# Kernel optimization log

Hardware: AMD Instinct MI355X
Metric: run time of the kernel (lower is better)

## Reference

```python
import jax, jax.numpy as jnp
import numpy as np

B, NB, NA, D, PF = 16384, 8, 16, 128, 1
IN_DIM = D + NA * D + D  # basis + flattened sf + task = 2304
QK_DIM = D * 3 * PF      # 384
V_DIM = D * PF           # 128


def rbf_similarity(x, y):
    # RBF kernel over the feature axis: exp(-0.5 * ||x - y||^2)
    return jnp.exp(-0.5 * jnp.sum((x - y) ** 2, axis=-1))


def setup_inputs() -> dict:
    key = jax.random.key(0)
    ks = jax.random.split(key, 9)
    basis = jax.random.normal(ks[0], (B, NB, D), dtype=jnp.float32)
    sf_all = jax.random.normal(ks[1], (B, NB, NA, D), dtype=jnp.float32)
    task = jax.random.normal(ks[2], (B, NB, D), dtype=jnp.float32)
    mask = (jax.random.uniform(ks[3], (B, NB, D * PF)) > 0.5).astype(jnp.float32)
    s_in = 1.0 / np.sqrt(IN_DIM)
    s_v = 1.0 / np.sqrt(D)
    Wq = jax.random.normal(ks[4], (IN_DIM, QK_DIM), dtype=jnp.float32) * s_in
    Wk = jax.random.normal(ks[5], (IN_DIM, QK_DIM), dtype=jnp.float32) * s_in
    bk = jnp.zeros((QK_DIM,), dtype=jnp.float32)
    Wv = jax.random.normal(ks[6], (D, V_DIM), dtype=jnp.float32) * s_v
    bv = jnp.zeros((V_DIM,), dtype=jnp.float32)
    return {"basis_features_all": basis, "sf_all": sf_all, "task": task, "mask": mask,
            "Wq": Wq, "Wk": Wk, "bk": bk, "Wv": Wv, "bv": bv}


def reference(basis_features_all, sf_all, task, mask, Wq, Wk, bk, Wv, bv):
    b = sf_all.shape[0]
    sf_all_r = jnp.reshape(sf_all, (b, NB, NA * D))          # (B, NB, NA*D)
    sf_first_r = sf_all_r[:, :1, :]                          # (B, 1, NA*D)
    task = jax.lax.stop_gradient(task)
    task_n = task / jnp.linalg.norm(task, ord=2, axis=-1, keepdims=True)

    # RBF similarity side-branch between consecutive beakers
    bst = jnp.concatenate([basis_features_all, sf_all_r, task_n], axis=-1)  # (B, NB, IN_DIM)
    sim = rbf_similarity(bst[:, :-1, :], bst[:, 1:, :]).mean(axis=0)        # (NB-1,)

    bf_first = basis_features_all[:, :1, :]
    bf_rest = jax.lax.stop_gradient(basis_features_all[:, 1:, :])
    bf_all = jnp.concatenate([bf_first, bf_rest], axis=1)

    q_in = jnp.concatenate([bf_first, sf_first_r, task_n[:, :1, :]], axis=-1)  # (B, 1, IN_DIM)
    query = q_in @ Wq                                                          # (B, 1, QK)
    k_in = jnp.concatenate([bf_all, sf_all_r, task_n], axis=-1)                # (B, NB, IN_DIM)
    keys = k_in @ Wk + bk                                                      # (B, NB, QK)
    values = sf_all @ Wv + bv                                                  # (B, NB, NA, V)

    mask_rep = jnp.repeat(mask, 3, axis=-1)                                    # (B, NB, QK)
    keys_masked = keys * mask_rep
    values_masked = values

    attn_logits = jnp.matmul(query, jnp.swapaxes(keys_masked, -2, -1)) / jnp.sqrt(jnp.float32(D * PF))
    attn_logits = jnp.where(attn_logits == 0, -1e9, attn_logits)               # zero-mask trick
    attention_weights = jax.nn.softmax(attn_logits, axis=-1)                   # (B, 1, NB)

    attended_sf = jnp.einsum('bna,baqf->bnqf', attention_weights, values_masked)  # (B, 1, NA, V)
    task_first = task[:, 0, :]                                                    # (B, D)
    q_1 = jnp.einsum('bi,bnji->bj', task_first, attended_sf)                      # (B, NA)
    return (q_1, attended_sf, attn_logits, attention_weights, keys_masked, values_masked, sim)
```

## Files before the change

kernel.cpp:

```cpp
#include <hip/hip_runtime.h>
#include <hip/hip_bf16.h>
#include <math.h>

static constexpr size_t OFF_ATT = 262144;
static constexpr size_t OFF_LOG = 33816576;
static constexpr size_t OFF_W   = 33947648;
static constexpr size_t OFF_KM  = 34078720;
static constexpr size_t OFF_VM  = 84410368;
static constexpr size_t OFF_SIM = 352845824;

typedef short bf16x8 __attribute__((ext_vector_type(8)));
typedef float f32x4 __attribute__((ext_vector_type(4)));

__device__ inline unsigned short f2bf(float f) {
  union { float f; unsigned u; } x; x.f = f;
  unsigned r = x.u + 0x7FFFu + ((x.u >> 16) & 1u);
  return (unsigned short)(r >> 16);
}

__device__ inline float wave_sum(float v) {
#pragma unroll
  for (int o = 32; o > 0; o >>= 1) v += __shfl_xor(v, o, 64);
  return v;
}

__global__ void norm_kernel(const float* __restrict__ task, float* __restrict__ invn,
                            float* __restrict__ simo) {
  int idx = blockIdx.x * 4 + (threadIdx.x >> 6);
  int lane = threadIdx.x & 63;
  float t0 = task[(size_t)idx * 128 + lane];
  float t1 = task[(size_t)idx * 128 + 64 + lane];
  float s = wave_sum(t0 * t0 + t1 * t1);
  if (lane == 0) invn[idx] = rsqrtf(s);
  if (blockIdx.x == 0 && threadIdx.x < 7) simo[threadIdx.x] = 0.0f;
}

__global__ void wprep_t(const float* __restrict__ W, unsigned short* __restrict__ WT,
                        int K, int N) {
  int ntn = N >> 6;
  int kt = blockIdx.x / ntn, nt = blockIdx.x % ntn;
  int k0 = kt * 64, n0 = nt * 64;
  __shared__ float t[64][65];
  int tid = threadIdx.x;
  int r = tid >> 2, c0 = (tid & 3) * 16;
#pragma unroll
  for (int q = 0; q < 4; ++q) {
    float4 v = *(const float4*)(W + (size_t)(k0 + r) * N + n0 + c0 + q * 4);
    t[r][c0 + q * 4 + 0] = v.x; t[r][c0 + q * 4 + 1] = v.y;
    t[r][c0 + q * 4 + 2] = v.z; t[r][c0 + q * 4 + 3] = v.w;
  }
  __syncthreads();
  int n = tid >> 2, kc0 = (tid & 3) * 16;
#pragma unroll
  for (int q = 0; q < 4; ++q) {
    int kc = kc0 + q * 4;
    ushort4 o = make_ushort4(f2bf(t[kc + 0][n]), f2bf(t[kc + 1][n]),
                             f2bf(t[kc + 2][n]), f2bf(t[kc + 3][n]));
    *(ushort4*)(WT + (size_t)(n0 + n) * K + k0 + kc) = o;
  }
}

__global__ __launch_bounds__(576) void abuild_sim(const float* __restrict__ basis,
                                                  const float* __restrict__ sf,
                                                  const float* __restrict__ task,
                                                  const float* __restrict__ invn,
                                                  unsigned short* __restrict__ Abf,
                                                  float* __restrict__ simo) {
  int b = blockIdx.x;
  int f = threadIdx.x;
  size_t row0 = (size_t)b * 8;
  float4 v[8];
#pragma unroll
  for (int n = 0; n < 8; ++n) {
    size_t row = row0 + n;
    float4 x;
    if (f < 32)       x = *(const float4*)(basis + row * 128 + f * 4);
    else if (f < 544) x = *(const float4*)(sf + row * 2048 + (f - 32) * 4);
    else {
      x = *(const float4*)(task + row * 128 + (f - 544) * 4);
      float s = invn[row];
      x.x *= s; x.y *= s; x.z *= s; x.w *= s;
    }
    v[n] = x;
    ushort4 o = make_ushort4(f2bf(x.x), f2bf(x.y), f2bf(x.z), f2bf(x.w));
    *(ushort4*)(Abf + row * 2304 + f * 4) = o;
  }
  float s7[7];
#pragma unroll
  for (int n = 1; n < 8; ++n) {
    float dx = v[n].x - v[n - 1].x, dy = v[n].y - v[n - 1].y;
    float dz = v[n].z - v[n - 1].z, dw = v[n].w - v[n - 1].w;
    s7[n - 1] = dx * dx + dy * dy + dz * dz + dw * dw;
  }
  __shared__ float red[9][7];
  int wid = threadIdx.x >> 6, lane = threadIdx.x & 63;
#pragma unroll
  for (int i = 0; i < 7; ++i) {
    float p = wave_sum(s7[i]);
    if (lane == 0) red[wid][i] = p;
  }
  __syncthreads();
  if (threadIdx.x < 7) {
    float s = 0.f;
#pragma unroll
    for (int w = 0; w < 9; ++w) s += red[w][threadIdx.x];
    atomicAdd(&simo[threadIdx.x], expf(-0.5f * s) * (1.0f / 16384.0f));
  }
}

template <int MODE>
__global__ __launch_bounds__(256) void qk_gemm(const unsigned short* __restrict__ Abf,
                                               const unsigned short* __restrict__ WT,
                                               const float* __restrict__ bias,
                                               const float* __restrict__ mask,
                                               float* __restrict__ outp) {
  __shared__ unsigned short As[2 * 4096];
  __shared__ unsigned short Bs[2 * 4096];
  int nwg = gridDim.x, per = nwg >> 3;
  int bid = blockIdx.x;
  int swz = (bid & 7) * per + (bid >> 3);
  int mt = swz / 3, nt = swz - mt * 3;
  int tid = threadIdx.x;
  int wave = tid >> 6, lane = tid & 63;
  int wr = wave >> 1, wc = wave & 1;
  int m0g = mt * 128, n0g = nt * 128;

  int c_lo = wave * 2 * 64 + lane;
  int row_q0 = c_lo >> 2, kc_q0 = (c_lo & 3) * 8;
  int c_hi = c_lo + 64;
  int row_q1 = c_hi >> 2, kc_q1 = (c_hi & 3) * 8;
  size_t ga_q0 = (MODE == 1) ? (size_t)(m0g + row_q0) * 8 : (size_t)(m0g + row_q0);
  size_t ga_q1 = (MODE == 1) ? (size_t)(m0g + row_q1) * 8 : (size_t)(m0g + row_q1);
  const unsigned short* ag0 = Abf + ga_q0 * 2304 + kc_q0;
  const unsigned short* ag1 = Abf + ga_q1 * 2304 + kc_q1;
  const unsigned short* bg0 = WT + (size_t)(n0g + row_q0) * 2304 + kc_q0;
  const unsigned short* bg1 = WT + (size_t)(n0g + row_q1) * 2304 + kc_q1;
  int ldsoff0 = wave * 2 * 512;
  int ldsoff1 = ldsoff0 + 512;

#define STAGE(ks, cur)                                                                   \
  do {                                                                                   \
    int _k0 = (ks) * 32;                                                                 \
    unsigned short* _a = As + (cur) * 4096;                                              \
    unsigned short* _b = Bs + (cur) * 4096;                                              \
    __builtin_amdgcn_global_load_lds(                                                    \
        (const __attribute__((address_space(1))) void*)(ag0 + _k0),                      \
        (__attribute__((address_space(3))) void*)(_a + ldsoff0), 16, 0, 0);              \
    __builtin_amdgcn_global_load_lds(                                                    \
        (const __attribute__((address_space(1))) void*)(ag1 + _k0),                      \
        (__attribute__((address_space(3))) void*)(_a + ldsoff1), 16, 0, 0);              \
    __builtin_amdgcn_global_load_lds(                                                    \
        (const __attribute__((address_space(1))) void*)(bg0 + _k0),                      \
        (__attribute__((address_space(3))) void*)(_b + ldsoff0), 16, 0, 0);              \
    __builtin_amdgcn_global_load_lds(                                                    \
        (const __attribute__((address_space(1))) void*)(bg1 + _k0),                      \
        (__attribute__((address_space(3))) void*)(_b + ldsoff1), 16, 0, 0);              \
  } while (0)

  f32x4 acc[4][4];
#pragma unroll
  for (int i = 0; i < 4; ++i)
#pragma unroll
    for (int j = 0; j < 4; ++j) acc[i][j] = (f32x4)(0.f);

  int la = lane & 15, lk = (lane >> 4) * 8;

  STAGE(0, 0);
  __syncthreads();
  int cur = 0;
  for (int ks = 0; ks < 72; ++ks) {
    if (ks < 71) STAGE(ks + 1, cur ^ 1);
    const unsigned short* aL = As + cur * 4096;
    const unsigned short* bL = Bs + cur * 4096;
    bf16x8 af[4], bf[4];
#pragma unroll
    for (int mi = 0; mi < 4; ++mi)
      af[mi] = *(const bf16x8*)(aL + (wr * 64 + mi * 16 + la) * 32 + lk);
#pragma unroll
    for (int ni = 0; ni < 4; ++ni)
      bf[ni] = *(const bf16x8*)(bL + (wc * 64 + ni * 16 + la) * 32 + lk);
#pragma unroll
    for (int mi = 0; mi < 4; ++mi)
#pragma unroll
      for (int ni = 0; ni < 4; ++ni)
        acc[mi][ni] = __builtin_amdgcn_mfma_f32_16x16x32_bf16(af[mi], bf[ni], acc[mi][ni], 0, 0, 0);
    __syncthreads();
    cur ^= 1;
  }
#undef STAGE

  int rq = lane >> 4;
#pragma unroll
  for (int mi = 0; mi < 4; ++mi) {
#pragma unroll
    for (int ni = 0; ni < 4; ++ni) {
      int colg = nt * 128 + wc * 64 + ni * 16 + la;
#pragma unroll
      for (int j = 0; j < 4; ++j) {
        int rowg = mt * 128 + wr * 64 + mi * 16 + rq * 4 + j;
        float v = acc[mi][ni][j];
        if (MODE == 0)
          v = (v + bias[colg]) * mask[(size_t)rowg * 128 + (unsigned)colg / 3u];
        outp[(size_t)rowg * 384 + colg] = v;
      }
    }
  }
}

__global__ void attn_kernel(const float* __restrict__ query, const float* __restrict__ km,
                            float* __restrict__ logits, float* __restrict__ wts) {
  int b = blockIdx.x;
  int tid = threadIdx.x;
  int w = tid >> 6, lane = tid & 63;
  __shared__ float lg[8];
  __shared__ float post[8];
  __shared__ float ex[8];
  for (int n = w; n < 8; n += 4) {
    float p = 0.f;
    for (int k = lane; k < 384; k += 64)
      p += query[(size_t)b * 384 + k] * km[((size_t)b * 8 + n) * 384 + k];
    p = wave_sum(p);
    if (lane == 0) lg[n] = p * 0.08838834764831845f;
  }
  __syncthreads();
  if (tid < 8) {
    float l = lg[tid];
    l = (l == 0.0f) ? -1e9f : l;
    post[tid] = l;
    logits[(size_t)b * 8 + tid] = l;
  }
  __syncthreads();
  if (tid < 8) {
    float m = post[0];
#pragma unroll
    for (int i = 1; i < 8; ++i) m = fmaxf(m, post[i]);
    ex[tid] = expf(post[tid] - m);
  }
  __syncthreads();
  if (tid < 8) {
    float s = 0.f;
#pragma unroll
    for (int i = 0; i < 8; ++i) s += ex[i];
    wts[(size_t)b * 8 + tid] = ex[tid] / s;
  }
}

__global__ __launch_bounds__(256) void v_gemm_attend(const float* __restrict__ sf,
                                                     const float* __restrict__ Wv,
                                                     const float* __restrict__ bv,
                                                     const float* __restrict__ wts,
                                                     const float* __restrict__ task,
                                                     float* __restrict__ vm,
                                                     float* __restrict__ att,
                                                     float* __restrict__ q1) {
  __shared__ unsigned short As[128 * 40];
  __shared__ unsigned short Bs[128 * 136];
  float* attL = (float*)As;
  int bid = blockIdx.x;
  int swz = (bid & 7) * 2048 + (bid >> 3);
  int b = swz;
  size_t m0 = (size_t)swz * 128;
  int tid = threadIdx.x;
  int wave = tid >> 6, lane = tid & 63;
  int wr = wave >> 1, wc = wave & 1;
  int r = tid >> 1, h = tid & 1;
  int la = lane & 15, lkq = lane >> 4;

#pragma unroll
  for (int q = 0; q < 16; ++q) {
    int flat = q * 256 + tid;
    int k = flat >> 5;
    int n4 = (flat & 31) * 4;
    float4 v = *(const float4*)(Wv + (size_t)k * 128 + n4);
    Bs[(n4 + 0) * 136 + k] = f2bf(v.x);
    Bs[(n4 + 1) * 136 + k] = f2bf(v.y);
    Bs[(n4 + 2) * 136 + k] = f2bf(v.z);
    Bs[(n4 + 3) * 136 + k] = f2bf(v.w);
  }

  f32x4 acc[4][4];
#pragma unroll
  for (int i = 0; i < 4; ++i)
#pragma unroll
    for (int j = 0; j < 4; ++j) acc[i][j] = (f32x4)(0.f);

  for (int ks = 0; ks < 4; ++ks) {
    int k0 = ks * 32;
    const float* ap = sf + (m0 + r) * 128 + k0 + h * 16;
    float4 v0 = *(const float4*)(ap);
    float4 v1 = *(const float4*)(ap + 4);
    float4 v2 = *(const float4*)(ap + 8);
    float4 v3 = *(const float4*)(ap + 12);
    ushort4 p0 = make_ushort4(f2bf(v0.x), f2bf(v0.y), f2bf(v0.z), f2bf(v0.w));
    ushort4 p1 = make_ushort4(f2bf(v1.x), f2bf(v1.y), f2bf(v1.z), f2bf(v1.w));
    ushort4 p2 = make_ushort4(f2bf(v2.x), f2bf(v2.y), f2bf(v2.z), f2bf(v2.w));
    ushort4 p3 = make_ushort4(f2bf(v3.x), f2bf(v3.y), f2bf(v3.z), f2bf(v3.w));
    *(ushort4*)(As + r * 40 + h * 16)      = p0;
    *(ushort4*)(As + r * 40 + h * 16 + 4)  = p1;
    *(ushort4*)(As + r * 40 + h * 16 + 8)  = p2;
    *(ushort4*)(As + r * 40 + h * 16 + 12) = p3;
    __syncthreads();
    bf16x8 af[4], bfr[4];
#pragma unroll
    for (int mi = 0; mi < 4; ++mi)
      af[mi] = *(const bf16x8*)(As + (wr * 64 + mi * 16 + la) * 40 + lkq * 8);
#pragma unroll
    for (int ni = 0; ni < 4; ++ni)
      bfr[ni] = *(const bf16x8*)(Bs + (wc * 64 + ni * 16 + la) * 136 + k0 + lkq * 8);
#pragma unroll
    for (int mi = 0; mi < 4; ++mi)
#pragma unroll
      for (int ni = 0; ni < 4; ++ni)
        acc[mi][ni] = __builtin_amdgcn_mfma_f32_16x16x32_bf16(af[mi], bfr[ni], acc[mi][ni], 0, 0, 0);
    __syncthreads();
  }

  float w4[4];
#pragma unroll
  for (int mi = 0; mi < 4; ++mi) w4[mi] = wts[(size_t)b * 8 + wr * 4 + mi];
  float pacc[4][4];
#pragma unroll
  for (int ni = 0; ni < 4; ++ni)
#pragma unroll
    for (int j = 0; j < 4; ++j) pacc[ni][j] = 0.f;
#pragma unroll
  for (int mi = 0; mi < 4; ++mi) {
#pragma unroll
    for (int ni = 0; ni < 4; ++ni) {
      int colg = wc * 64 + ni * 16 + la;
      float bb = bv[colg];
#pragma unroll
      for (int j = 0; j < 4; ++j) {
        size_t rowg = m0 + wr * 64 + mi * 16 + lkq * 4 + j;
        float v = acc[mi][ni][j] + bb;
        vm[rowg * 128 + colg] = v;
        pacc[ni][j] = fmaf(w4[mi], v, pacc[ni][j]);
      }
    }
  }
  if (wr == 0) {
#pragma unroll
    for (int ni = 0; ni < 4; ++ni)
#pragma unroll
      for (int j = 0; j < 4; ++j)
        attL[(lkq * 4 + j) * 132 + wc * 64 + ni * 16 + la] = pacc[ni][j];
  }
  __syncthreads();
  if (wr == 1) {
#pragma unroll
    for (int ni = 0; ni < 4; ++ni)
#pragma unroll
      for (int j = 0; j < 4; ++j)
        attL[(lkq * 4 + j) * 132 + wc * 64 + ni * 16 + la] += pacc[ni][j];
  }
  __syncthreads();
#pragma unroll
  for (int i = 0; i < 2; ++i) {
    int fidx = tid + i * 256;
    int a = fidx >> 5, c = (fidx & 31) * 4;
    f32x4 vv = *(const f32x4*)(attL + a * 132 + c);
    *(f32x4*)(att + (size_t)b * 2048 + a * 128 + c) = vv;
  }
  for (int j = wave; j < 16; j += 4) {
    float p = task[(size_t)b * 1024 + lane] * attL[j * 132 + lane]
            + task[(size_t)b * 1024 + 64 + lane] * attL[j * 132 + 64 + lane];
    p = wave_sum(p);
    if (lane == 0) q1[(size_t)b * 16 + j] = p;
  }
}

extern "C" void kernel_launch(void* const* d_in, const int* in_sizes, int n_in,
                              void* d_out, int out_size, void* d_ws, size_t ws_size,
                              hipStream_t stream) {
  const float* basis = (const float*)d_in[0];
  const float* sf    = (const float*)d_in[1];
  const float* task  = (const float*)d_in[2];
  const float* mask  = (const float*)d_in[3];
  const float* Wq    = (const float*)d_in[4];
  const float* Wk    = (const float*)d_in[5];
  const float* bk    = (const float*)d_in[6];
  const float* Wv    = (const float*)d_in[7];
  const float* bv    = (const float*)d_in[8];

  float* out  = (float*)d_out;
  float* q1   = out;
  float* att  = out + OFF_ATT;
  float* logi = out + OFF_LOG;
  float* wts  = out + OFF_W;
  float* km   = out + OFF_KM;
  float* vm   = out + OFF_VM;
  float* simo = out + OFF_SIM;

  float* query = att;
  float* invn  = att + 6291456;
  unsigned short* WkT = (unsigned short*)(att + 6422528);
  unsigned short* WqT = WkT + 884736;
  unsigned short* Abf = (unsigned short*)vm;

  norm_kernel<<<32768, 256, 0, stream>>>(task, invn, simo);
  wprep_t<<<216, 256, 0, stream>>>(Wk, WkT, 2304, 384);
  wprep_t<<<216, 256, 0, stream>>>(Wq, WqT, 2304, 384);
  abuild_sim<<<16384, 576, 0, stream>>>(basis, sf, task, invn, Abf, simo);
  qk_gemm<0><<<3072, 256, 0, stream>>>(Abf, WkT, bk, mask, km);
  qk_gemm<1><<<384, 256, 0, stream>>>(Abf, WqT, nullptr, nullptr, query);
  attn_kernel<<<16384, 256, 0, stream>>>(query, km, logi, wts);
  v_gemm_attend<<<16384, 256, 0, stream>>>(sf, Wv, bv, wts, task, vm, att, q1);
}
```

Before: 1.401 ms.

## Reuse bf16 A-matrix from workspace in value GEMM and batch attention per wave

When a large enough workspace is available, the bf16 packed input matrix, transposed weights, query and norms move into that workspace, so the value GEMM can read the already-converted bf16 sf slice instead of re-reading fp32 sf and converting it. Wv is also pre-transposed to bf16 once, so each block copies it with vector loads instead of scattered transposing stores. The attention kernel now gives each wave one batch row with register-held query and no shared memory or block barriers. The risk is that the workspace path only runs when ws_size is large enough, otherwise the old path is used.

```diff
diff --git a/kernel.cpp b/kernel.cpp
--- a/kernel.cpp
+++ b/kernel.cpp
@@ -207,46 +207,48 @@
   }
 }
 
-__global__ void attn_kernel(const float* __restrict__ query, const float* __restrict__ km,
-                            float* __restrict__ logits, float* __restrict__ wts) {
-  int b = blockIdx.x;
-  int tid = threadIdx.x;
-  int w = tid >> 6, lane = tid & 63;
-  __shared__ float lg[8];
-  __shared__ float post[8];
-  __shared__ float ex[8];
-  for (int n = w; n < 8; n += 4) {
+__global__ __launch_bounds__(256) void attn_kernel4(const float* __restrict__ query,
+                                                    const float* __restrict__ km,
+                                                    float* __restrict__ logits,
+                                                    float* __restrict__ wts) {
+  int w = threadIdx.x >> 6, lane = threadIdx.x & 63;
+  int b = blockIdx.x * 4 + w;
+  float q[6];
+#pragma unroll
+  for (int j = 0; j < 6; ++j) q[j] = query[(size_t)b * 384 + lane + 64 * j];
+  float lg[8];
+#pragma unroll
+  for (int n = 0; n < 8; ++n) {
+    const float* kr = km + ((size_t)b * 8 + n) * 384;
     float p = 0.f;
-    for (int k = lane; k < 384; k += 64)
-      p += query[(size_t)b * 384 + k] * km[((size_t)b * 8 + n) * 384 + k];
+#pragma unroll
+    for (int j = 0; j < 6; ++j) p = fmaf(q[j], kr[lane + 64 * j], p);
     p = wave_sum(p);
-    if (lane == 0) lg[n] = p * 0.08838834764831845f;
-  }
-  __syncthreads();
-  if (tid < 8) {
-    float l = lg[tid];
-    l = (l == 0.0f) ? -1e9f : l;
-    post[tid] = l;
-    logits[(size_t)b * 8 + tid] = l;
-  }
-  __syncthreads();
-  if (tid < 8) {
-    float m = post[0];
-#pragma unroll
-    for (int i = 1; i < 8; ++i) m = fmaxf(m, post[i]);
-    ex[tid] = expf(post[tid] - m);
-  }
-  __syncthreads();
-  if (tid < 8) {
-    float s = 0.f;
-#pragma unroll
-    for (int i = 0; i < 8; ++i) s += ex[i];
-    wts[(size_t)b * 8 + tid] = ex[tid] / s;
-  }
-}
-
+    float l = p * 0.08838834764831845f;
+    lg[n] = (l == 0.0f) ? -1e9f : l;
+  }
+  float m = lg[0];
+#pragma unroll
+  for (int i = 1; i < 8; ++i) m = fmaxf(m, lg[i]);
+  float ex[8], s = 0.f;
+#pragma unroll
+  for (int i = 0; i < 8; ++i) { ex[i] = expf(lg[i] - m); s += ex[i]; }
+  float inv = 1.0f / s;
+  if (lane < 8) {
+    float lv = lg[0], ev = ex[0];
+#pragma unroll
+    for (int i = 1; i < 8; ++i)
+      if (lane == i) { lv = lg[i]; ev = ex[i]; }
+    logits[(size_t)b * 8 + lane] = lv;
+    wts[(size_t)b * 8 + lane] = ev * inv;
+  }
+}
+
+template <int ABF>
 __global__ __launch_bounds__(256) void v_gemm_attend(const float* __restrict__ sf,
+                                                     const unsigned short* __restrict__ Abf,
                                                      const float* __restrict__ Wv,
+                                                     const unsigned short* __restrict__ WvT,
                                                      const float* __restrict__ bv,
                                                      const float* __restrict__ wts,
                                                      const float* __restrict__ task,
@@ -266,16 +268,30 @@
   int r = tid >> 1, h = tid & 1;
   int la = lane & 15, lkq = lane >> 4;
 
-#pragma unroll
-  for (int q = 0; q < 16; ++q) {
-    int flat = q * 256 + tid;
-    int k = flat >> 5;
-    int n4 = (flat & 31) * 4;
-    float4 v = *(const float4*)(Wv + (size_t)k * 128 + n4);
-    Bs[(n4 + 0) * 136 + k] = f2bf(v.x);
-    Bs[(n4 + 1) * 136 + k] = f2bf(v.y);
-    Bs[(n4 + 2) * 136 + k] = f2bf(v.z);
-    Bs[(n4 + 3) * 136 + k] = f2bf(v.w);
+  if (ABF) {
+#pragma unroll
+    for (int q = 0; q < 8; ++q) {
+      bf16x8 v = *(const bf16x8*)(WvT + (size_t)r * 128 + h * 64 + q * 8);
+      *(bf16x8*)(Bs + r * 136 + h * 64 + q * 8) = v;
+    }
+  } else {
+#pragma unroll
+    for (int q = 0; q < 16; ++q) {
+      int flat = q * 256 + tid;
+      int k = flat >> 5;
+      int n4 = (flat & 31) * 4;
+      float4 v = *(const float4*)(Wv + (size_t)k * 128 + n4);
+      Bs[(n4 + 0) * 136 + k] = f2bf(v.x);
+      Bs[(n4 + 1) * 136 + k] = f2bf(v.y);
+      Bs[(n4 + 2) * 136 + k] = f2bf(v.z);
+      Bs[(n4 + 3) * 136 + k] = f2bf(v.w);
+    }
+  }
+
+  const unsigned short* abase = nullptr;
+  if (ABF) {
+    int n = r >> 4, a = r & 15;
+    abase = Abf + ((size_t)b * 8 + n) * 2304 + 128 + (size_t)a * 128 + h * 16;
   }
 
   f32x4 acc[4][4];
@@ -286,19 +302,26 @@
 
   for (int ks = 0; ks < 4; ++ks) {
     int k0 = ks * 32;
-    const float* ap = sf + (m0 + r) * 128 + k0 + h * 16;
-    float4 v0 = *(const float4*)(ap);
-    float4 v1 = *(const float4*)(ap + 4);
-    float4 v2 = *(const float4*)(ap + 8);
-    float4 v3 = *(const float4*)(ap + 12);
-    ushort4 p0 = make_ushort4(f2bf(v0.x), f2bf(v0.y), f2bf(v0.z), f2bf(v0.w));
-    ushort4 p1 = make_ushort4(f2bf(v1.x), f2bf(v1.y), f2bf(v1.z), f2bf(v1.w));
-    ushort4 p2 = make_ushort4(f2bf(v2.x), f2bf(v2.y), f2bf(v2.z), f2bf(v2.w));
-    ushort4 p3 = make_ushort4(f2bf(v3.x), f2bf(v3.y), f2bf(v3.z), f2bf(v3.w));
-    *(ushort4*)(As + r * 40 + h * 16)      = p0;
-    *(ushort4*)(As + r * 40 + h * 16 + 4)  = p1;
-    *(ushort4*)(As + r * 40 + h * 16 + 8)  = p2;
-    *(ushort4*)(As + r * 40 + h * 16 + 12) = p3;
+    if (ABF) {
+      bf16x8 u0 = *(const bf16x8*)(abase + k0);
+      bf16x8 u1 = *(const bf16x8*)(abase + k0 + 8);
+      *(bf16x8*)(As + r * 40 + h * 16)     = u0;
+      *(bf16x8*)(As + r * 40 + h * 16 + 8) = u1;
+    } else {
+      const float* ap = sf + (m0 + r) * 128 + k0 + h * 16;
+      float4 v0 = *(const float4*)(ap);
+      float4 v1 = *(const float4*)(ap + 4);
+      float4 v2 = *(const float4*)(ap + 8);
+      float4 v3 = *(const float4*)(ap + 12);
+      ushort4 p0 = make_ushort4(f2bf(v0.x), f2bf(v0.y), f2bf(v0.z), f2bf(v0.w));
+      ushort4 p1 = make_ushort4(f2bf(v1.x), f2bf(v1.y), f2bf(v1.z), f2bf(v1.w));
+      ushort4 p2 = make_ushort4(f2bf(v2.x), f2bf(v2.y), f2bf(v2.z), f2bf(v2.w));
+      ushort4 p3 = make_ushort4(f2bf(v3.x), f2bf(v3.y), f2bf(v3.z), f2bf(v3.w));
+      *(ushort4*)(As + r * 40 + h * 16)      = p0;
+      *(ushort4*)(As + r * 40 + h * 16 + 4)  = p1;
+      *(ushort4*)(As + r * 40 + h * 16 + 8)  = p2;
+      *(ushort4*)(As + r * 40 + h * 16 + 12) = p3;
+    }
     __syncthreads();
     bf16x8 af[4], bfr[4];
 #pragma unroll
@@ -391,18 +414,38 @@
   float* vm   = out + OFF_VM;
   float* simo = out + OFF_SIM;
 
-  float* query = att;
-  float* invn  = att + 6291456;
-  unsigned short* WkT = (unsigned short*)(att + 6422528);
-  unsigned short* WqT = WkT + 884736;
-  unsigned short* Abf = (unsigned short*)vm;
+  constexpr size_t WS_NEED = 603979776ull + 1769472ull + 1769472ull + 32768ull +
+                             25165824ull + 524288ull;
+  bool usews = ws_size >= WS_NEED;
+
+  unsigned short *Abf, *WkT, *WqT, *WvT = nullptr;
+  float *query, *invn;
+  if (usews) {
+    unsigned char* ws = (unsigned char*)d_ws;
+    Abf   = (unsigned short*)ws;
+    WkT   = (unsigned short*)(ws + 603979776ull);
+    WqT   = (unsigned short*)(ws + 605749248ull);
+    WvT   = (unsigned short*)(ws + 607518720ull);
+    query = (float*)(ws + 607551488ull);
+    invn  = (float*)(ws + 632717312ull);
+  } else {
+    query = att;
+    invn  = att + 6291456;
+    WkT   = (unsigned short*)(att + 6422528);
+    WqT   = WkT + 884736;
+    Abf   = (unsigned short*)vm;
+  }
 
   norm_kernel<<<32768, 256, 0, stream>>>(task, invn, simo);
   wprep_t<<<216, 256, 0, stream>>>(Wk, WkT, 2304, 384);
   wprep_t<<<216, 256, 0, stream>>>(Wq, WqT, 2304, 384);
+  if (usews) wprep_t<<<4, 256, 0, stream>>>(Wv, WvT, 128, 128);
   abuild_sim<<<16384, 576, 0, stream>>>(basis, sf, task, invn, Abf, simo);
   qk_gemm<0><<<3072, 256, 0, stream>>>(Abf, WkT, bk, mask, km);
   qk_gemm<1><<<384, 256, 0, stream>>>(Abf, WqT, nullptr, nullptr, query);
-  attn_kernel<<<16384, 256, 0, stream>>>(query, km, logi, wts);
-  v_gemm_attend<<<16384, 256, 0, stream>>>(sf, Wv, bv, wts, task, vm, att, q1);
-}
+  attn_kernel4<<<4096, 256, 0, stream>>>(query, km, logi, wts);
+  if (usews)
+    v_gemm_attend<1><<<16384, 256, 0, stream>>>(sf, Abf, Wv, WvT, bv, wts, task, vm, att, q1);
+  else
+    v_gemm_attend<0><<<16384, 256, 0, stream>>>(sf, Abf, Wv, WvT, bv, wts, task, vm, att, q1);
+}
```

Result: faster. 1.310 ms (-6.5%).
